# Kernel optimization log

Hardware: AMD Instinct MI355X
Metric: run time of the kernel (lower is better)

The kernel has to match this reference:

```python
import jax, jax.numpy as jnp
import numpy as np

N = 300000   # number of occupied voxels (sparse tensor rows)
L = 100      # grid side length -> 1e6 cells, occupancy 0.3
C = 32       # channels (channelwise/depthwise conv)
KS = 3       # kernel_size per axis
D = 3        # spatial dimension
R = (KS - 1) // 2


def _build_sparse_structure():
    """Sample N unique voxel coords and build kernel maps (edge lists) like
    MinkowskiEngine's coordinate manager: for each kernel offset, pairs
    (in_idx, out_idx) such that coords[in_idx] == coords[out_idx] + offset."""
    rng = np.random.default_rng(0)
    flat = rng.choice(L ** 3, size=N, replace=False)
    coords = np.stack([flat // (L * L), (flat // L) % L, flat % L], axis=1).astype(np.int32)
    keys = flat.astype(np.int64)
    order = np.argsort(keys)
    sk = keys[order]
    out_ids = np.arange(N, dtype=np.int64)
    in_list, out_list = [], []
    for dx in range(-R, R + 1):
        for dy in range(-R, R + 1):
            for dz in range(-R, R + 1):
                nx = coords[:, 0].astype(np.int64) + dx
                ny = coords[:, 1].astype(np.int64) + dy
                nz = coords[:, 2].astype(np.int64) + dz
                inb = (nx >= 0) & (nx < L) & (ny >= 0) & (ny < L) & (nz >= 0) & (nz < L)
                nk = (nx * L + ny) * L + nz
                pos = np.searchsorted(sk, nk)
                pos_c = np.clip(pos, 0, N - 1)
                ok = inb & (sk[pos_c] == nk)
                in_list.append(order[pos_c[ok]])
                out_list.append(out_ids[ok])
    in_idx = np.concatenate(in_list).astype(np.int32)
    out_idx = np.concatenate(out_list).astype(np.int32)
    return coords, in_idx, out_idx


def setup_inputs() -> dict:
    coords, in_idx, out_idx = _build_sparse_structure()
    key = jax.random.key(0)
    k1, k2 = jax.random.split(key)
    in_feats = jax.random.normal(k1, (N, C), dtype=jnp.float32)
    kernel = jax.random.normal(k2, (KS ** D, C), dtype=jnp.float32)  # depthwise kernel
    return {
        "coords": jnp.asarray(coords),
        "in_idx": jnp.asarray(in_idx),
        "out_idx": jnp.asarray(out_idx),
        "in_feats": in_feats,
        "kernel": kernel,
    }


def reference(coords, in_idx, out_idx, in_feats, kernel):
    # index_array = KS ** flip(arange(D)) -> [9, 3, 1] for KS=3, D=3
    index_pow = jnp.array([KS ** (D - 1 - i) for i in range(D)], dtype=jnp.int32)
    # tensor_stride = 1; kernel_coord = (C_in - C_out)//1 + (KS-1)//2, per edge [E, D]
    kernel_coord = coords[in_idx] - coords[out_idx] + R
    k1d = jnp.sum(index_pow[None, :] * kernel_coord, axis=1)  # [E] in [0, KS**D)
    # gather-multiply-scatter: out_F[out] += in_feats[in] * kernel[k1d]
    out_F = jnp.zeros_like(in_feats).at[out_idx].add(in_feats[in_idx] * kernel[k1d])
    return out_F
```

## Files before the change

kernel.cpp:

```cpp
#include <hip/hip_runtime.h>

#define NCH 32
#define GROUPS 8
#define KVOL 27
#define LG 100
#define LP 102
#define RGN 5
#define NRGN 20
#define NREGIONS (NRGN * NRGN * NRGN)
#define BSIDE 7
#define BVOL 343
#define CELLS 125

__global__ void build_dense(const int* __restrict__ coords,
                            int* __restrict__ dense, int N) {
    int i = blockIdx.x * blockDim.x + threadIdx.x;
    if (i >= N) return;
    int x = coords[3 * i + 0];
    int y = coords[3 * i + 1];
    int z = coords[3 * i + 2];
    dense[((size_t)(x + 1) * LP + (y + 1)) * LP + (z + 1)] = i + 1;
}

__global__ __launch_bounds__(256, 8) void gather_conv_region(
        const int* __restrict__ dense,
        const float4* __restrict__ in_feats4,
        const float4* __restrict__ kernel4,
        float4* __restrict__ out4) {
    __shared__ float4 kw[(KVOL + 1) * GROUPS];
    __shared__ int brick[BVOL];
    __shared__ unsigned bitcol[49];
    __shared__ int qmeta[CELLS];
    __shared__ unsigned qmask[CELLS];
    __shared__ int smap[CELLS];
    __shared__ unsigned koff[KVOL + 1];
    __shared__ int hist[7];
    __shared__ int nint;

    int tid = threadIdx.x;
    int g   = tid & 7;

    if (tid == 0) nint = 0;
    if (tid < 7) hist[tid] = 0;
    if (tid < 49) bitcol[tid] = 0;
    if (tid < KVOL + 1) {
        int k = tid;
        int dx = 1, dy = 1, dz = 1;
        if (k < KVOL) { dx = k / 9; dy = (k / 3) % 3; dz = k % 3; }
        int off = dx * 49 + dy * 7 + dz;
        koff[tid] = ((unsigned)(k * 128) << 7) | (unsigned)off;
    }
    if (tid < (KVOL + 1) * GROUPS) {
        int kr = tid >> 3;
        kw[tid] = (kr < KVOL) ? kernel4[tid]
                              : make_float4(0.f, 0.f, 0.f, 0.f);
    }

    int b = blockIdx.x;
    int r = (b & 7) * (NREGIONS >> 3) + (b >> 3);
    int bx = r / (NRGN * NRGN);
    int by = (r / NRGN) % NRGN;
    int bz = r % NRGN;
    int ox = bx * RGN, oy = by * RGN, oz = bz * RGN;

    for (int i = tid; i < BVOL; i += 256) {
        int lx = i / 49, ly = (i / 7) % 7, lz = i % 7;
        int v = dense[((size_t)(ox + lx) * LP + (oy + ly)) * LP + (oz + lz)];
        brick[i] = v;
        if (v) {
            atomicOr(&bitcol[lx * 7 + ly], 1u << lz);
            if ((unsigned)(lx - 1) < RGN && (unsigned)(ly - 1) < RGN &&
                (unsigned)(lz - 1) < RGN) {
                int p = atomicAdd(&nint, 1);
                qmeta[p] = lx | (ly << 3) | (lz << 6) | (i << 9);
            }
        }
    }
    __syncthreads();

    int n = nint;

    if (tid < n) {
        int m0 = qmeta[tid];
        int lx = m0 & 7, ly = (m0 >> 3) & 7, lz = (m0 >> 6) & 7;
        int colbase = (lx - 1) * 7 + (ly - 1);
        unsigned mask = 0;
        #pragma unroll
        for (int dx = 0; dx < 3; ++dx)
            #pragma unroll
            for (int dy = 0; dy < 3; ++dy) {
                unsigned c = (bitcol[colbase + dx * 7 + dy] >> (lz - 1)) & 7u;
                mask |= c << (dx * 9 + dy * 3);
            }
        qmask[tid] = mask;
        int nb = (__popc(mask) + 3) >> 2;
        int h = atomicAdd(&hist[nb - 1], 1);
        qmeta[tid] = m0 | (nb << 18) | (h << 22);
    }
    __syncthreads();

    if (tid < n) {
        int m0 = qmeta[tid];
        int nb = (m0 >> 18) & 15;
        int pos = m0 >> 22;
        #pragma unroll
        for (int bb = 1; bb < 7; ++bb)
            if (bb >= nb) pos += hist[bb];
        int s = pos;
        if (pos < (n & ~31))
            s = (pos & ~31) | ((pos >> 2) & 7) | ((pos & 3) << 3);
        smap[s] = (tid << 5) | nb;
    }
    __syncthreads();

    const char* kwb = (const char*)kw + (g << 4);
    int lr = tid >> 3;
    for (int base = 0; base < n; base += 32) {
        int lo = base + lr;
        if (lo < n) {
            int d     = smap[lo];
            int q     = d >> 5;
            int nb    = d & 31;
            int m0    = qmeta[q];
            int cell  = (m0 >> 9) & 511;
            int cellb = cell - 57;
            int orow  = brick[cell] - 1;
            unsigned m = qmask[q];
            float4 acc = make_float4(0.f, 0.f, 0.f, 0.f);
            for (int t = 0; t < nb; ++t) {
                int k0 = m ? __builtin_ctz(m) : KVOL; m &= m - 1;
                int k1 = m ? __builtin_ctz(m) : KVOL; m &= m - 1;
                int k2 = m ? __builtin_ctz(m) : KVOL; m &= m - 1;
                int k3 = m ? __builtin_ctz(m) : KVOL; m &= m - 1;
                unsigned o0 = koff[k0], o1 = koff[k1];
                unsigned o2 = koff[k2], o3 = koff[k3];
                int v0 = brick[cellb + (int)(o0 & 127u)];
                int v1 = brick[cellb + (int)(o1 & 127u)];
                int v2 = brick[cellb + (int)(o2 & 127u)];
                int v3 = brick[cellb + (int)(o3 & 127u)];
                float4 f0 = in_feats4[(size_t)(v0 - 1) * GROUPS + g];
                float4 f1 = in_feats4[(size_t)(v1 - 1) * GROUPS + g];
                float4 f2 = in_feats4[(size_t)(v2 - 1) * GROUPS + g];
                float4 f3 = in_feats4[(size_t)(v3 - 1) * GROUPS + g];
                float4 w0 = *(const float4*)(kwb + (o0 >> 7));
                float4 w1 = *(const float4*)(kwb + (o1 >> 7));
                float4 w2 = *(const float4*)(kwb + (o2 >> 7));
                float4 w3 = *(const float4*)(kwb + (o3 >> 7));
                acc.x += f0.x * w0.x; acc.y += f0.y * w0.y;
                acc.z += f0.z * w0.z; acc.w += f0.w * w0.w;
                acc.x += f1.x * w1.x; acc.y += f1.y * w1.y;
                acc.z += f1.z * w1.z; acc.w += f1.w * w1.w;
                acc.x += f2.x * w2.x; acc.y += f2.y * w2.y;
                acc.z += f2.z * w2.z; acc.w += f2.w * w2.w;
                acc.x += f3.x * w3.x; acc.y += f3.y * w3.y;
                acc.z += f3.z * w3.z; acc.w += f3.w * w3.w;
            }
            out4[(size_t)orow * GROUPS + g] = acc;
        }
    }
}

__global__ void mink_conv_scatter(const int* __restrict__ coords,
                                  const int* __restrict__ in_idx,
                                  const int* __restrict__ out_idx,
                                  const float4* __restrict__ in_feats4,
                                  const float4* __restrict__ kernel4,
                                  float* __restrict__ out,
                                  int E) {
    __shared__ float4 kws[KVOL * GROUPS];
    for (int i = threadIdx.x; i < KVOL * GROUPS; i += blockDim.x)
        kws[i] = kernel4[i];
    __syncthreads();
    int t = blockIdx.x * blockDim.x + threadIdx.x;
    if (t >= E * GROUPS) return;
    int e = t >> 3, g = t & 7;
    int vi = in_idx[e], vo = out_idx[e];
    int c0 = coords[vi * 3 + 0] - coords[vo * 3 + 0] + 1;
    int c1 = coords[vi * 3 + 1] - coords[vo * 3 + 1] + 1;
    int c2 = coords[vi * 3 + 2] - coords[vo * 3 + 2] + 1;
    int k1d = (c0 * 3 + c1) * 3 + c2;
    float4 f = in_feats4[vi * GROUPS + g];
    float4 w = kws[k1d * GROUPS + g];
    float* o = out + vo * NCH + g * 4;
    atomicAdd(o + 0, f.x * w.x);
    atomicAdd(o + 1, f.y * w.y);
    atomicAdd(o + 2, f.z * w.z);
    atomicAdd(o + 3, f.w * w.w);
}

extern "C" void kernel_launch(void* const* d_in, const int* in_sizes, int n_in,
                              void* d_out, int out_size, void* d_ws, size_t ws_size,
                              hipStream_t stream) {
    const int*   coords   = (const int*)d_in[0];
    const int*   in_idx   = (const int*)d_in[1];
    const int*   out_idx  = (const int*)d_in[2];
    const float* in_feats = (const float*)d_in[3];
    const float* kernel   = (const float*)d_in[4];

    const int E     = in_sizes[1];
    const int Nrows = out_size / NCH;

    const size_t dense_bytes = (size_t)LP * LP * LP * sizeof(int);

    if (ws_size >= dense_bytes) {
        int* dense = (int*)d_ws;
        hipMemsetAsync(dense, 0, dense_bytes, stream);

        int block = 256;
        int grid1 = (Nrows + block - 1) / block;
        build_dense<<<grid1, block, 0, stream>>>(coords, dense, Nrows);

        gather_conv_region<<<NREGIONS, 256, 0, stream>>>(
            dense, (const float4*)in_feats, (const float4*)kernel,
            (float4*)d_out);
    } else {
        hipMemsetAsync(d_out, 0, (size_t)out_size * sizeof(float), stream);
        int total = E * GROUPS;
        int block = 256;
        int grid  = (total + block - 1) / block;
        mink_conv_scatter<<<grid, block, 0, stream>>>(
            coords, in_idx, out_idx,
            (const float4*)in_feats, (const float4*)kernel,
            (float*)d_out, E);
    }
}
```

Before: 136.6 us.

## Stage region halo features into shared memory before depthwise gather-convolution

Each block now compacts the occupied cells of its 7x7x7 brick into slots and loads their features once, coalesced, into an LDS buffer. The inner loop then reads neighbour features from shared memory instead of issuing scattered global gathers. Per-output metadata is packed into a uint4 table so the compute loop reads one record per output. A fallback path keeps using global gathers when a brick has more than 128 occupied cells. The larger shared footprint lowers the launch-bounds occupancy target from 8 to 6 blocks per CU.

```diff
diff --git a/kernel.cpp b/kernel.cpp
--- a/kernel.cpp
+++ b/kernel.cpp
@@ -11,6 +11,7 @@
 #define BSIDE 7
 #define BVOL 343
 #define CELLS 125
+#define SLOTS 128
 
 __global__ void build_dense(const int* __restrict__ coords,
                             int* __restrict__ dense, int N) {
@@ -22,25 +23,27 @@
     dense[((size_t)(x + 1) * LP + (y + 1)) * LP + (z + 1)] = i + 1;
 }
 
-__global__ __launch_bounds__(256, 8) void gather_conv_region(
+__global__ __launch_bounds__(256, 6) void gather_conv_region(
         const int* __restrict__ dense,
         const float4* __restrict__ in_feats4,
         const float4* __restrict__ kernel4,
         float4* __restrict__ out4) {
     __shared__ float4 kw[(KVOL + 1) * GROUPS];
+    __shared__ float4 feat[SLOTS * GROUPS];
     __shared__ int brick[BVOL];
+    __shared__ int slotrow[BVOL + 1];
     __shared__ unsigned bitcol[49];
+    __shared__ unsigned qmask[CELLS];
     __shared__ int qmeta[CELLS];
-    __shared__ unsigned qmask[CELLS];
-    __shared__ int smap[CELLS];
+    __shared__ uint4 sAB[CELLS];
     __shared__ unsigned koff[KVOL + 1];
     __shared__ int hist[7];
-    __shared__ int nint;
+    __shared__ int nslots, nint;
 
     int tid = threadIdx.x;
     int g   = tid & 7;
 
-    if (tid == 0) nint = 0;
+    if (tid == 0) { nslots = 0; nint = 0; }
     if (tid < 7) hist[tid] = 0;
     if (tid < 49) bitcol[tid] = 0;
     if (tid < KVOL + 1) {
@@ -66,96 +69,152 @@
     for (int i = tid; i < BVOL; i += 256) {
         int lx = i / 49, ly = (i / 7) % 7, lz = i % 7;
         int v = dense[((size_t)(ox + lx) * LP + (oy + ly)) * LP + (oz + lz)];
-        brick[i] = v;
-        if (v) {
+        int s = 0;
+        if (v > 0) {
+            s = atomicAdd(&nslots, 1);
+            slotrow[s] = v - 1;
             atomicOr(&bitcol[lx * 7 + ly], 1u << lz);
             if ((unsigned)(lx - 1) < RGN && (unsigned)(ly - 1) < RGN &&
                 (unsigned)(lz - 1) < RGN) {
                 int p = atomicAdd(&nint, 1);
-                qmeta[p] = lx | (ly << 3) | (lz << 6) | (i << 9);
-            }
+                qmeta[p] = i;
+            }
+            s += 1;
         }
-    }
-    __syncthreads();
-
-    int n = nint;
+        brick[i] = s;
+    }
+    __syncthreads();
+
+    int ns = nslots;
+    int n  = nint;
+    bool ovf = (ns > SLOTS);
+
+    {
+        int lim = ovf ? SLOTS : ns;
+        for (int s = tid >> 3; s < lim; s += 32)
+            feat[s * GROUPS + g] = in_feats4[(size_t)slotrow[s] * GROUPS + g];
+    }
 
     if (tid < n) {
-        int m0 = qmeta[tid];
-        int lx = m0 & 7, ly = (m0 >> 3) & 7, lz = (m0 >> 6) & 7;
-        int colbase = (lx - 1) * 7 + (ly - 1);
+        int cell = qmeta[tid] & 511;
+        int lx = cell / 49, ly = (cell / 7) % 7, lz = cell % 7;
+        int cb = (lx - 1) * 7 + (ly - 1);
         unsigned mask = 0;
         #pragma unroll
         for (int dx = 0; dx < 3; ++dx)
             #pragma unroll
             for (int dy = 0; dy < 3; ++dy) {
-                unsigned c = (bitcol[colbase + dx * 7 + dy] >> (lz - 1)) & 7u;
+                unsigned c = (bitcol[cb + dx * 7 + dy] >> (lz - 1)) & 7u;
                 mask |= c << (dx * 9 + dy * 3);
             }
         qmask[tid] = mask;
         int nb = (__popc(mask) + 3) >> 2;
         int h = atomicAdd(&hist[nb - 1], 1);
-        qmeta[tid] = m0 | (nb << 18) | (h << 22);
+        qmeta[tid] = cell | (nb << 9) | (h << 13);
     }
     __syncthreads();
 
     if (tid < n) {
         int m0 = qmeta[tid];
-        int nb = (m0 >> 18) & 15;
-        int pos = m0 >> 22;
+        int cell = m0 & 511;
+        int nb = (m0 >> 9) & 15;
+        int pos = m0 >> 13;
         #pragma unroll
         for (int bb = 1; bb < 7; ++bb)
             if (bb >= nb) pos += hist[bb];
         int s = pos;
         if (pos < (n & ~31))
             s = (pos & ~31) | ((pos >> 2) & 7) | ((pos & 3) << 3);
-        smap[s] = (tid << 5) | nb;
+        int orow = slotrow[brick[cell] - 1];
+        sAB[s] = make_uint4(qmask[tid], (unsigned)orow,
+                            (unsigned)cell, (unsigned)nb);
     }
     __syncthreads();
 
     const char* kwb = (const char*)kw + (g << 4);
+    const char* ftb = (const char*)feat + (g << 4);
     int lr = tid >> 3;
-    for (int base = 0; base < n; base += 32) {
-        int lo = base + lr;
-        if (lo < n) {
-            int d     = smap[lo];
-            int q     = d >> 5;
-            int nb    = d & 31;
-            int m0    = qmeta[q];
-            int cell  = (m0 >> 9) & 511;
-            int cellb = cell - 57;
-            int orow  = brick[cell] - 1;
-            unsigned m = qmask[q];
-            float4 acc = make_float4(0.f, 0.f, 0.f, 0.f);
-            for (int t = 0; t < nb; ++t) {
-                int k0 = m ? __builtin_ctz(m) : KVOL; m &= m - 1;
-                int k1 = m ? __builtin_ctz(m) : KVOL; m &= m - 1;
-                int k2 = m ? __builtin_ctz(m) : KVOL; m &= m - 1;
-                int k3 = m ? __builtin_ctz(m) : KVOL; m &= m - 1;
-                unsigned o0 = koff[k0], o1 = koff[k1];
-                unsigned o2 = koff[k2], o3 = koff[k3];
-                int v0 = brick[cellb + (int)(o0 & 127u)];
-                int v1 = brick[cellb + (int)(o1 & 127u)];
-                int v2 = brick[cellb + (int)(o2 & 127u)];
-                int v3 = brick[cellb + (int)(o3 & 127u)];
-                float4 f0 = in_feats4[(size_t)(v0 - 1) * GROUPS + g];
-                float4 f1 = in_feats4[(size_t)(v1 - 1) * GROUPS + g];
-                float4 f2 = in_feats4[(size_t)(v2 - 1) * GROUPS + g];
-                float4 f3 = in_feats4[(size_t)(v3 - 1) * GROUPS + g];
-                float4 w0 = *(const float4*)(kwb + (o0 >> 7));
-                float4 w1 = *(const float4*)(kwb + (o1 >> 7));
-                float4 w2 = *(const float4*)(kwb + (o2 >> 7));
-                float4 w3 = *(const float4*)(kwb + (o3 >> 7));
-                acc.x += f0.x * w0.x; acc.y += f0.y * w0.y;
-                acc.z += f0.z * w0.z; acc.w += f0.w * w0.w;
-                acc.x += f1.x * w1.x; acc.y += f1.y * w1.y;
-                acc.z += f1.z * w1.z; acc.w += f1.w * w1.w;
-                acc.x += f2.x * w2.x; acc.y += f2.y * w2.y;
-                acc.z += f2.z * w2.z; acc.w += f2.w * w2.w;
-                acc.x += f3.x * w3.x; acc.y += f3.y * w3.y;
-                acc.z += f3.z * w3.z; acc.w += f3.w * w3.w;
-            }
-            out4[(size_t)orow * GROUPS + g] = acc;
+    if (!ovf) {
+        for (int base = 0; base < n; base += 32) {
+            int lo = base + lr;
+            if (lo < n) {
+                uint4 R = sAB[lo];
+                unsigned m = R.x;
+                int orow   = (int)R.y;
+                int cellb  = (int)R.z - 57;
+                int nb     = (int)R.w;
+                float4 acc = make_float4(0.f, 0.f, 0.f, 0.f);
+                for (int t = 0; t < nb; ++t) {
+                    int k0 = m ? __builtin_ctz(m) : KVOL; m &= m - 1;
+                    int k1 = m ? __builtin_ctz(m) : KVOL; m &= m - 1;
+                    int k2 = m ? __builtin_ctz(m) : KVOL; m &= m - 1;
+                    int k3 = m ? __builtin_ctz(m) : KVOL; m &= m - 1;
+                    unsigned o0 = koff[k0], o1 = koff[k1];
+                    unsigned o2 = koff[k2], o3 = koff[k3];
+                    int s0 = brick[cellb + (int)(o0 & 127u)] - 1;
+                    int s1 = brick[cellb + (int)(o1 & 127u)] - 1;
+                    int s2 = brick[cellb + (int)(o2 & 127u)] - 1;
+                    int s3 = brick[cellb + (int)(o3 & 127u)] - 1;
+                    float4 f0 = *(const float4*)(ftb + (s0 << 7));
+                    float4 f1 = *(const float4*)(ftb + (s1 << 7));
+                    float4 f2 = *(const float4*)(ftb + (s2 << 7));
+                    float4 f3 = *(const float4*)(ftb + (s3 << 7));
+                    float4 w0 = *(const float4*)(kwb + (o0 >> 7));
+                    float4 w1 = *(const float4*)(kwb + (o1 >> 7));
+                    float4 w2 = *(const float4*)(kwb + (o2 >> 7));
+                    float4 w3 = *(const float4*)(kwb + (o3 >> 7));
+                    acc.x += f0.x * w0.x; acc.y += f0.y * w0.y;
+                    acc.z += f0.z * w0.z; acc.w += f0.w * w0.w;
+                    acc.x += f1.x * w1.x; acc.y += f1.y * w1.y;
+                    acc.z += f1.z * w1.z; acc.w += f1.w * w1.w;
+                    acc.x += f2.x * w2.x; acc.y += f2.y * w2.y;
+                    acc.z += f2.z * w2.z; acc.w += f2.w * w2.w;
+                    acc.x += f3.x * w3.x; acc.y += f3.y * w3.y;
+                    acc.z += f3.z * w3.z; acc.w += f3.w * w3.w;
+                }
+                out4[(size_t)orow * GROUPS + g] = acc;
+            }
+        }
+    } else {
+        for (int base = 0; base < n; base += 32) {
+            int lo = base + lr;
+            if (lo < n) {
+                uint4 R = sAB[lo];
+                unsigned m = R.x;
+                int orow   = (int)R.y;
+                int cellb  = (int)R.z - 57;
+                int nb     = (int)R.w;
+                float4 acc = make_float4(0.f, 0.f, 0.f, 0.f);
+                for (int t = 0; t < nb; ++t) {
+                    int k0 = m ? __builtin_ctz(m) : KVOL; m &= m - 1;
+                    int k1 = m ? __builtin_ctz(m) : KVOL; m &= m - 1;
+                    int k2 = m ? __builtin_ctz(m) : KVOL; m &= m - 1;
+                    int k3 = m ? __builtin_ctz(m) : KVOL; m &= m - 1;
+                    unsigned o0 = koff[k0], o1 = koff[k1];
+                    unsigned o2 = koff[k2], o3 = koff[k3];
+                    int r0 = slotrow[brick[cellb + (int)(o0 & 127u)] - 1];
+                    int r1 = slotrow[brick[cellb + (int)(o1 & 127u)] - 1];
+                    int r2 = slotrow[brick[cellb + (int)(o2 & 127u)] - 1];
+                    int r3 = slotrow[brick[cellb + (int)(o3 & 127u)] - 1];
+                    float4 f0 = in_feats4[(size_t)r0 * GROUPS + g];
+                    float4 f1 = in_feats4[(size_t)r1 * GROUPS + g];
+                    float4 f2 = in_feats4[(size_t)r2 * GROUPS + g];
+                    float4 f3 = in_feats4[(size_t)r3 * GROUPS + g];
+                    float4 w0 = *(const float4*)(kwb + (o0 >> 7));
+                    float4 w1 = *(const float4*)(kwb + (o1 >> 7));
+                    float4 w2 = *(const float4*)(kwb + (o2 >> 7));
+                    float4 w3 = *(const float4*)(kwb + (o3 >> 7));
+                    acc.x += f0.x * w0.x; acc.y += f0.y * w0.y;
+                    acc.z += f0.z * w0.z; acc.w += f0.w * w0.w;
+                    acc.x += f1.x * w1.x; acc.y += f1.y * w1.y;
+                    acc.z += f1.z * w1.z; acc.w += f1.w * w1.w;
+                    acc.x += f2.x * w2.x; acc.y += f2.y * w2.y;
+                    acc.z += f2.z * w2.z; acc.w += f2.w * w2.w;
+                    acc.x += f3.x * w3.x; acc.y += f3.y * w3.y;
+                    acc.z += f3.z * w3.z; acc.w += f3.w * w3.w;
+                }
+                out4[(size_t)orow * GROUPS + g] = acc;
+            }
         }
     }
 }
```

New measurement: 140.4 us. +2.8%, slower.
